# Performance work log

Measured on AMD Instinct MI355X. Metric: run time of the kernel, lower is better.

The kernel has to match this reference:

```python
import jax, jax.numpy as jnp
import numpy as np

K_SIZE = 3
PAD = (K_SIZE - 1) // 2


def setup_inputs() -> dict:
    key = jax.random.key(0)
    k1, k2, k3, k4 = jax.random.split(key, 4)
    b, c, h, w = 16, 2048, 56, 56
    return {
        "x": jax.random.normal(k1, (b, c, h, w), dtype=jnp.float32),
        "w_offset": jax.random.normal(k2, (K_SIZE, 1, K_SIZE), dtype=jnp.float32),
        "w_deform": jax.random.normal(k3, (K_SIZE,), dtype=jnp.float32),
        "b_deform": jax.random.normal(k4, (1,), dtype=jnp.float32),
    }


def _dca_forward(x, w_offset, w_deform, b_deform):
    b, c, h, w = x.shape
    # global average pool -> per-channel descriptor (b, c)
    y = x.mean(axis=(2, 3))
    # offset prediction: Conv1d(1 -> k, kernel=k, pad=(k-1)//2, no bias) over channel axis
    offsets = jax.lax.conv_general_dilated(
        y[:, None, :],              # (b, 1, c)
        w_offset,                   # (k_out=K, in=1, kw=K)
        window_strides=(1,),
        padding=[(PAD, PAD)],
        dimension_numbers=("NCH", "OIH", "NCH"),
    )                               # (b, K, c)
    # deformable 1D conv along channel axis with linear interpolation
    idx = jnp.arange(c, dtype=jnp.float32)                    # (c,)
    taps = jnp.arange(K_SIZE, dtype=jnp.float32) - PAD        # (K,)
    p = idx[None, None, :] + taps[None, :, None] + offsets    # (b, K, c)
    p = jnp.clip(p, 0.0, c - 1.0)
    p0 = jnp.floor(p)
    frac = p - p0
    p0i = p0.astype(jnp.int32)
    p1i = jnp.minimum(p0i + 1, c - 1)
    yb = jnp.broadcast_to(y[:, None, :], p0i.shape)           # (b, K, c)
    v0 = jnp.take_along_axis(yb, p0i, axis=2)
    v1 = jnp.take_along_axis(yb, p1i, axis=2)
    sampled = v0 * (1.0 - frac) + v1 * frac                   # (b, K, c)
    y_local = jnp.einsum("bkc,k->bc", sampled, w_deform) + b_deform  # (b, c)
    gate = jax.nn.sigmoid(y_local)
    return x * gate[:, :, None, None]


def reference(x, w_offset, w_deform, b_deform):
    return _dca_forward(x, w_offset, w_deform, b_deform)
```

## Files before the change

### kernel.cpp

```cpp
#include <hip/hip_runtime.h>

#define BATCH 16
#define CH    2048
#define HW    3136
#define HW4   784

__global__ __launch_bounds__(256) void mean_kernel(const float* __restrict__ x,
                                                   float* __restrict__ y) {
    const int plane = blockIdx.x;
    const float4* xp = reinterpret_cast<const float4*>(x) + (size_t)plane * HW4;

    float sum = 0.0f;
    for (int i = threadIdx.x; i < HW4; i += 256) {
        float4 v = xp[i];
        sum += (v.x + v.y) + (v.z + v.w);
    }
    #pragma unroll
    for (int o = 32; o > 0; o >>= 1) sum += __shfl_down(sum, o, 64);

    __shared__ float part[4];
    const int lane = threadIdx.x & 63;
    const int wid  = threadIdx.x >> 6;
    if (lane == 0) part[wid] = sum;
    __syncthreads();
    if (threadIdx.x == 0) {
        float s = (part[0] + part[1]) + (part[2] + part[3]);
        y[plane] = s * (1.0f / (float)HW);
    }
}

__global__ __launch_bounds__(256) void gate_kernel(const float* __restrict__ y,
                                                   const float* __restrict__ w_offset,
                                                   const float* __restrict__ w_deform,
                                                   const float* __restrict__ b_deform,
                                                   float* __restrict__ gate) {
    __shared__ float ly[CH];
    const int b = blockIdx.x;
    for (int i = threadIdx.x; i < CH; i += 256) ly[i] = y[b * CH + i];
    __syncthreads();

    float wo[9];
    #pragma unroll
    for (int i = 0; i < 9; ++i) wo[i] = w_offset[i];
    const float wd0 = w_deform[0], wd1 = w_deform[1], wd2 = w_deform[2];
    const float bd  = b_deform[0];

    for (int c = threadIdx.x; c < CH; c += 256) {
        const float ym = (c >= 1)      ? ly[c - 1] : 0.0f;
        const float y0 = ly[c];
        const float yp = (c < CH - 1)  ? ly[c + 1] : 0.0f;

        float acc = 0.0f;
        #pragma unroll
        for (int k = 0; k < 3; ++k) {
            const float off = ym * wo[k * 3 + 0] + y0 * wo[k * 3 + 1] + yp * wo[k * 3 + 2];
            float p = (float)c + (float)(k - 1) + off;
            p = fminf(fmaxf(p, 0.0f), (float)(CH - 1));
            const float p0 = floorf(p);
            const float fr = p - p0;
            const int i0 = (int)p0;
            const int i1 = min(i0 + 1, CH - 1);
            const float s = ly[i0] * (1.0f - fr) + ly[i1] * fr;
            const float wk = (k == 0) ? wd0 : (k == 1) ? wd1 : wd2;
            acc += s * wk;
        }
        const float v = acc + bd;
        gate[b * CH + c] = 1.0f / (1.0f + expf(-v));
    }
}

__global__ __launch_bounds__(256) void scale_kernel(const float* __restrict__ x,
                                                    const float* __restrict__ gate,
                                                    float* __restrict__ out) {
    const int plane = blockIdx.x;
    const float g = gate[plane];
    const float4* xp = reinterpret_cast<const float4*>(x)   + (size_t)plane * HW4;
    float4*       op = reinterpret_cast<float4*>(out)       + (size_t)plane * HW4;
    for (int i = threadIdx.x; i < HW4; i += 256) {
        float4 v = xp[i];
        v.x *= g; v.y *= g; v.z *= g; v.w *= g;
        op[i] = v;
    }
}

extern "C" void kernel_launch(void* const* d_in, const int* in_sizes, int n_in,
                              void* d_out, int out_size, void* d_ws, size_t ws_size,
                              hipStream_t stream) {
    const float* x        = (const float*)d_in[0];
    const float* w_offset = (const float*)d_in[1];
    const float* w_deform = (const float*)d_in[2];
    const float* b_deform = (const float*)d_in[3];
    float* out = (float*)d_out;

    float* y    = (float*)d_ws;
    float* gate = y + (size_t)BATCH * CH;

    mean_kernel<<<BATCH * CH, 256, 0, stream>>>(x, y);
    gate_kernel<<<BATCH, 256, 0, stream>>>(y, w_offset, w_deform, b_deform, gate);
    scale_kernel<<<BATCH * CH, 256, 0, stream>>>(x, gate, out);
}
```

Measured before the change: 236.6 us.

## Fuse gate computation into scale kernel, reverse plane order, nontemporal stores

Removes the separate gate kernel: each scale block has thread 0 compute its plane's sigmoid gate directly from the pooled means, shared through LDS. Planes are processed in reverse order so the most recently read tail of x (still in cache from the mean pass) is consumed first. Output stores use nontemporal hints to avoid polluting cache. Adds a serial per-block gate computation and barrier before streaming.

```diff
diff --git a/kernel.cpp b/kernel.cpp
--- a/kernel.cpp
+++ b/kernel.cpp
@@ -1,18 +1,21 @@
 #include <hip/hip_runtime.h>
 
-#define BATCH 16
-#define CH    2048
-#define HW    3136
-#define HW4   784
+#define BATCH   16
+#define CH      2048
+#define HW      3136
+#define HW4     784
+#define NPLANES (BATCH * CH)
+
+typedef float v4f __attribute__((ext_vector_type(4)));
 
 __global__ __launch_bounds__(256) void mean_kernel(const float* __restrict__ x,
                                                    float* __restrict__ y) {
     const int plane = blockIdx.x;
-    const float4* xp = reinterpret_cast<const float4*>(x) + (size_t)plane * HW4;
+    const v4f* xp = reinterpret_cast<const v4f*>(x) + (size_t)plane * HW4;
 
     float sum = 0.0f;
     for (int i = threadIdx.x; i < HW4; i += 256) {
-        float4 v = xp[i];
+        v4f v = xp[i];
         sum += (v.x + v.y) + (v.z + v.w);
     }
     #pragma unroll
@@ -29,57 +32,51 @@
     }
 }
 
-__global__ __launch_bounds__(256) void gate_kernel(const float* __restrict__ y,
-                                                   const float* __restrict__ w_offset,
-                                                   const float* __restrict__ w_deform,
-                                                   const float* __restrict__ b_deform,
-                                                   float* __restrict__ gate) {
-    __shared__ float ly[CH];
-    const int b = blockIdx.x;
-    for (int i = threadIdx.x; i < CH; i += 256) ly[i] = y[b * CH + i];
-    __syncthreads();
+__global__ __launch_bounds__(256) void scale_kernel(const float* __restrict__ x,
+                                                    const float* __restrict__ y,
+                                                    const float* __restrict__ w_offset,
+                                                    const float* __restrict__ w_deform,
+                                                    const float* __restrict__ b_deform,
+                                                    float* __restrict__ out) {
+    const int plane = (NPLANES - 1) - (int)blockIdx.x;
+    __shared__ float sgate;
 
-    float wo[9];
-    #pragma unroll
-    for (int i = 0; i < 9; ++i) wo[i] = w_offset[i];
-    const float wd0 = w_deform[0], wd1 = w_deform[1], wd2 = w_deform[2];
-    const float bd  = b_deform[0];
+    if (threadIdx.x == 0) {
+        const int b = plane >> 11;
+        const int c = plane & (CH - 1);
+        const float* yb = y + b * CH;
 
-    for (int c = threadIdx.x; c < CH; c += 256) {
-        const float ym = (c >= 1)      ? ly[c - 1] : 0.0f;
-        const float y0 = ly[c];
-        const float yp = (c < CH - 1)  ? ly[c + 1] : 0.0f;
+        const float ym = (c >= 1)      ? yb[c - 1] : 0.0f;
+        const float y0 = yb[c];
+        const float yp = (c < CH - 1)  ? yb[c + 1] : 0.0f;
 
         float acc = 0.0f;
         #pragma unroll
         for (int k = 0; k < 3; ++k) {
-            const float off = ym * wo[k * 3 + 0] + y0 * wo[k * 3 + 1] + yp * wo[k * 3 + 2];
+            const float off = ym * w_offset[k * 3 + 0]
+                            + y0 * w_offset[k * 3 + 1]
+                            + yp * w_offset[k * 3 + 2];
             float p = (float)c + (float)(k - 1) + off;
             p = fminf(fmaxf(p, 0.0f), (float)(CH - 1));
             const float p0 = floorf(p);
             const float fr = p - p0;
             const int i0 = (int)p0;
             const int i1 = min(i0 + 1, CH - 1);
-            const float s = ly[i0] * (1.0f - fr) + ly[i1] * fr;
-            const float wk = (k == 0) ? wd0 : (k == 1) ? wd1 : wd2;
-            acc += s * wk;
+            const float s = yb[i0] * (1.0f - fr) + yb[i1] * fr;
+            acc += s * w_deform[k];
         }
-        const float v = acc + bd;
-        gate[b * CH + c] = 1.0f / (1.0f + expf(-v));
+        const float v = acc + b_deform[0];
+        sgate = 1.0f / (1.0f + expf(-v));
     }
-}
+    __syncthreads();
+    const float g = sgate;
 
-__global__ __launch_bounds__(256) void scale_kernel(const float* __restrict__ x,
-                                                    const float* __restrict__ gate,
-                                                    float* __restrict__ out) {
-    const int plane = blockIdx.x;
-    const float g = gate[plane];
-    const float4* xp = reinterpret_cast<const float4*>(x)   + (size_t)plane * HW4;
-    float4*       op = reinterpret_cast<float4*>(out)       + (size_t)plane * HW4;
+    const v4f* xp = reinterpret_cast<const v4f*>(x)   + (size_t)plane * HW4;
+    v4f*       op = reinterpret_cast<v4f*>(out)       + (size_t)plane * HW4;
     for (int i = threadIdx.x; i < HW4; i += 256) {
-        float4 v = xp[i];
-        v.x *= g; v.y *= g; v.z *= g; v.w *= g;
-        op[i] = v;
+        v4f v = xp[i];
+        v *= g;
+        __builtin_nontemporal_store(v, &op[i]);
     }
 }
 
@@ -92,10 +89,8 @@
     const float* b_deform = (const float*)d_in[3];
     float* out = (float*)d_out;
 
-    float* y    = (float*)d_ws;
-    float* gate = y + (size_t)BATCH * CH;
+    float* y = (float*)d_ws;
 
-    mean_kernel<<<BATCH * CH, 256, 0, stream>>>(x, y);
-    gate_kernel<<<BATCH, 256, 0, stream>>>(y, w_offset, w_deform, b_deform, gate);
-    scale_kernel<<<BATCH * CH, 256, 0, stream>>>(x, gate, out);
+    mean_kernel<<<NPLANES, 256, 0, stream>>>(x, y);
+    scale_kernel<<<NPLANES, 256, 0, stream>>>(x, y, w_offset, w_deform, b_deform, out);
 }
```

Measured after the change: 193.8 us, median of 2. 18.1% less time.
